# Optimization experiments

Hardware: AMD Instinct MI355X
Metric: run time of the kernel (lower is better)

## Reference

```python
import jax, jax.numpy as jnp
import numpy as np

N = 50000      # nodes
E = 400000     # edges
D = 512        # embed_dim
L = 3          # num gcn layers
INNER = (L + 1) * D
EPS = 1e-5     # BatchNorm1d eps


def setup_inputs() -> dict:
    key = jax.random.key(0)
    ks = jax.random.split(key, 6)
    x = jax.random.normal(ks[0], (N, D), dtype=jnp.float32)
    edge_index = jax.random.randint(ks[1], (2, E), 0, N, dtype=jnp.int64)
    Ws = jax.random.normal(ks[2], (L, D, D), dtype=jnp.float32) / np.float32(np.sqrt(D))
    bs = jnp.zeros((L, D), jnp.float32)
    bn_gamma = jnp.ones((INNER,), jnp.float32)
    bn_beta = jnp.zeros((INNER,), jnp.float32)
    out_W = jax.random.normal(ks[3], (INNER, D), dtype=jnp.float32) / np.float32(np.sqrt(INNER))
    out_b = jnp.zeros((D,), jnp.float32)
    return {"x": x, "edge_index": edge_index, "Ws": Ws, "bs": bs,
            "bn_gamma": bn_gamma, "bn_beta": bn_beta, "out_W": out_W, "out_b": out_b}


def _gcn_conv(x, W, b, src, dst):
    # PyG GCNConv: add self-loops, sym-normalize, aggregate source->target.
    h = x @ W                                            # [N, D]
    deg = jnp.zeros((N,), x.dtype).at[dst].add(1.0) + 1.0  # in-degree + self-loop
    dinv = jax.lax.rsqrt(deg)
    norm = dinv[src] * dinv[dst]                         # [E]
    agg = jnp.zeros_like(h).at[dst].add(h[src] * norm[:, None])
    agg = agg + h * (dinv * dinv)[:, None]               # self-loop messages
    return agg + b


def reference(x, edge_index, Ws, bs, bn_gamma, bn_beta, out_W, out_b):
    src, dst = edge_index[0], edge_index[1]
    h = x
    x_cat = [x]
    for l in range(L):                                   # fixed small layer loop
        h = jax.nn.gelu(_gcn_conv(h, Ws[l], bs[l], src, dst), approximate=False)
        x_cat.append(h)
    xc = jnp.concatenate(x_cat, axis=-1)                 # [N, (L+1)*D]
    # BatchNorm1d, training-mode batch statistics (biased variance)
    mean = jnp.mean(xc, axis=0)
    var = jnp.var(xc, axis=0)
    xn = (xc - mean) * jax.lax.rsqrt(var + EPS) * bn_gamma + bn_beta
    return xn @ out_W + out_b                            # [N, D]
```

## Files before the change

### kernel.cpp

```cpp
#include <hip/hip_runtime.h>
#include <math.h>

#define N_NODES 50000
#define N_EDGES 400000
#define DIM 512
#define NLAYER 3
#define INNER 2048
#define BN_EPS 1e-5f
#define MPAD 50048

typedef unsigned short u16;
typedef unsigned int u32;

typedef __attribute__((ext_vector_type(8))) short bf16x8;
typedef __attribute__((ext_vector_type(4))) float f32x4;

__device__ __forceinline__ u16 f2bf(float f) {
  union { float f; u32 u; } v; v.f = f;
  u32 u = v.u;
  u32 r = (u + 0x7FFFu + ((u >> 16) & 1u)) >> 16;
  return (u16)r;
}
__device__ __forceinline__ float bf2f(u16 h) {
  union { u32 u; float f; } v; v.u = ((u32)h) << 16; return v.f;
}

#define GLOAD_LDS16(g, l)                                                       \
  __builtin_amdgcn_global_load_lds(                                             \
      (const __attribute__((address_space(1))) u32*)(g),                        \
      (__attribute__((address_space(3))) u32*)(l), 16, 0, 0)


__global__ void k_deg(const int* __restrict__ ei, int* __restrict__ deg) {
  int e = blockIdx.x * blockDim.x + threadIdx.x;
  if (e < N_EDGES) atomicAdd(&deg[ei[N_EDGES + e]], 1);
}

__global__ void k_dinv(const int* __restrict__ deg, float* __restrict__ dinv) {
  int i = blockIdx.x * blockDim.x + threadIdx.x;
  if (i < N_NODES) dinv[i] = rsqrtf((float)(deg[i] + 1));
}

__global__ __launch_bounds__(1024) void k_scan1(const int* __restrict__ deg,
                                                int* __restrict__ bsum, int n) {
  __shared__ int wsum[16];
  int tid = threadIdx.x;
  int lane = tid & 63, wv = tid >> 6;
  int i = blockIdx.x * 1024 + tid;
  int x = (i < n) ? deg[i] : 0;
#pragma unroll
  for (int d = 1; d < 64; d <<= 1) x += __shfl_xor(x, d, 64);
  if (lane == 0) wsum[wv] = x;
  __syncthreads();
  if (tid == 0) {
    int s = 0;
#pragma unroll
    for (int k = 0; k < 16; k++) s += wsum[k];
    bsum[blockIdx.x] = s;
  }
}

__global__ void k_scan2(int* __restrict__ bsum, int* __restrict__ offs, int nb) {
  int lane = threadIdx.x;
  int v = (lane < nb) ? bsum[lane] : 0;
  int x = v;
#pragma unroll
  for (int d = 1; d < 64; d <<= 1) {
    int y = __shfl_up(x, d, 64);
    if (lane >= d) x += y;
  }
  if (lane < nb) bsum[lane] = x - v;
  if (lane == nb - 1) offs[N_NODES] = x;
}

__global__ __launch_bounds__(1024) void k_scan3(const int* __restrict__ deg,
                                                const int* __restrict__ bsum,
                                                int* __restrict__ offs, int n) {
  __shared__ int wsum[16];
  int tid = threadIdx.x;
  int lane = tid & 63, wv = tid >> 6;
  int i = blockIdx.x * 1024 + tid;
  int v = (i < n) ? deg[i] : 0;
  int x = v;
#pragma unroll
  for (int d = 1; d < 64; d <<= 1) {
    int y = __shfl_up(x, d, 64);
    if (lane >= d) x += y;
  }
  if (lane == 63) wsum[wv] = x;
  __syncthreads();
  if (wv == 0) {
    int w = (lane < 16) ? wsum[lane] : 0;
#pragma unroll
    for (int d = 1; d < 16; d <<= 1) {
      int y = __shfl_up(w, d, 64);
      if (lane >= d) w += y;
    }
    if (lane < 16) wsum[lane] = w;
  }
  __syncthreads();
  if (i < n) offs[i] = bsum[blockIdx.x] + (wv ? wsum[wv - 1] : 0) + x - v;
}

__global__ void k_fill(const int* __restrict__ ei, const int* __restrict__ offs,
                       int* __restrict__ cursor, const float* __restrict__ dinv,
                       int* __restrict__ csr_src, float* __restrict__ csr_norm) {
  int e = blockIdx.x * blockDim.x + threadIdx.x;
  if (e >= N_EDGES) return;
  int s = ei[e];
  int d = ei[N_EDGES + e];
  int p = atomicAdd(&cursor[d], 1);
  int idx = offs[d] + p;
  csr_src[idx] = s;
  csr_norm[idx] = dinv[s] * dinv[d];
}

__global__ void k_convert(const float* __restrict__ src, u16* __restrict__ xcat, int n4) {
  int i = blockIdx.x * blockDim.x + threadIdx.x;
  if (i >= n4) return;
  float4 v = ((const float4*)src)[i];
  uint2 o;
  o.x = (u32)f2bf(v.x) | ((u32)f2bf(v.y) << 16);
  o.y = (u32)f2bf(v.z) | ((u32)f2bf(v.w) << 16);
  int row = i >> 7;
  int c4 = (i & 127) * 4;
  *(uint2*)(xcat + (size_t)row * INNER + c4) = o;
}

__global__ __launch_bounds__(256) void k_transpose_tiled(
    const float* __restrict__ W, const float* __restrict__ scale,
    u16* __restrict__ WT, int K) {
  __shared__ float tile[32][33];
  int k0 = blockIdx.x * 32, j0 = blockIdx.y * 32;
  int c = threadIdx.x & 31, r8 = threadIdx.x >> 5;
#pragma unroll
  for (int rr = 0; rr < 4; rr++) {
    int row = rr * 8 + r8;
    float v = W[(size_t)(k0 + row) * DIM + j0 + c];
    if (scale) v *= scale[k0 + row];
    tile[row][c] = v;
  }
  __syncthreads();
#pragma unroll
  for (int rr = 0; rr < 4; rr++) {
    int row = rr * 8 + r8;
    WT[(size_t)(j0 + row) * K + k0 + c] = f2bf(tile[c][row]);
  }
}

#define BM 128
#define BN 128
#define BK 32

__global__ __launch_bounds__(256) void gemm_bt(
    const u16* __restrict__ A, int lda,
    const u16* __restrict__ Bt, const float* __restrict__ bias,
    float* __restrict__ Cf, u16* __restrict__ Cb, int M, int K) {
  __shared__ __align__(16) u16 As[BM * BK];
  __shared__ __align__(16) u16 Bs[BN * BK];
  int tid = threadIdx.x;

  int Mblocks = gridDim.y;
  int flat = blockIdx.y * gridDim.x + blockIdx.x;
  int g = flat >> 5;
  int r = flat & 31;
  int P = Mblocks - (g << 3);
  P = (P > 8) ? 8 : P;
  int mb = (g << 3) + r % P;
  int nb = r / P;
  int m0 = mb * BM;
  int n0 = nb * BN;

  int wave = tid >> 6, lane = tid & 63;
  int wm = (wave & 1) * 64, wn = (wave >> 1) * 64;
  int lr = lane & 15;
  int lq = lane >> 4;
  int ric = lane >> 2;
  int seg = (lane & 3) * 8;

  const u16* ap0 = A + (size_t)(m0 + wave * 32 + ric) * lda + seg;
  const u16* ap1 = ap0 + (size_t)16 * lda;
  const u16* bp0 = Bt + (size_t)(n0 + wave * 32 + ric) * K + seg;
  const u16* bp1 = bp0 + (size_t)16 * K;
  u16* asl0 = &As[(wave * 2) * 512];
  u16* asl1 = asl0 + 512;
  u16* bsl0 = &Bs[(wave * 2) * 512];
  u16* bsl1 = bsl0 + 512;

  f32x4 acc[4][4];
#pragma unroll
  for (int i = 0; i < 4; i++)
#pragma unroll
    for (int j = 0; j < 4; j++) acc[i][j] = (f32x4){0.f, 0.f, 0.f, 0.f};

  for (int k0 = 0; k0 < K; k0 += BK) {
    GLOAD_LDS16(ap0, asl0);
    GLOAD_LDS16(ap1, asl1);
    GLOAD_LDS16(bp0, bsl0);
    GLOAD_LDS16(bp1, bsl1);
    ap0 += BK; ap1 += BK; bp0 += BK; bp1 += BK;
    __syncthreads();
    bf16x8 af[4], bfr[4];
#pragma unroll
    for (int i = 0; i < 4; i++)
      af[i] = *(const bf16x8*)(&As[(wm + i * 16 + lr) * BK + lq * 8]);
#pragma unroll
    for (int j = 0; j < 4; j++)
      bfr[j] = *(const bf16x8*)(&Bs[(wn + j * 16 + lr) * BK + lq * 8]);
#pragma unroll
    for (int i = 0; i < 4; i++)
#pragma unroll
      for (int j = 0; j < 4; j++)
        acc[i][j] = __builtin_amdgcn_mfma_f32_16x16x32_bf16(af[i], bfr[j], acc[i][j], 0, 0, 0);
    __syncthreads();
  }
#pragma unroll
  for (int i = 0; i < 4; i++) {
    int row_b = m0 + wm + i * 16 + lq * 4;
#pragma unroll
    for (int j = 0; j < 4; j++) {
      int col = n0 + wn + j * 16 + lr;
      if (Cf) {
        float bv = bias ? bias[col] : 0.f;
#pragma unroll
        for (int r2 = 0; r2 < 4; r2++) {
          int row = row_b + r2;
          if (row < M) Cf[(size_t)row * DIM + col] = acc[i][j][r2] + bv;
        }
      } else {
#pragma unroll
        for (int r2 = 0; r2 < 4; r2++)
          Cb[(size_t)(row_b + r2) * DIM + col] = f2bf(acc[i][j][r2]);
      }
    }
  }
}

__device__ __forceinline__ void accum8(float* a, uint4 h, float w) {
  a[0] += w * bf2f((u16)(h.x & 0xffffu));
  a[1] += w * bf2f((u16)(h.x >> 16));
  a[2] += w * bf2f((u16)(h.y & 0xffffu));
  a[3] += w * bf2f((u16)(h.y >> 16));
  a[4] += w * bf2f((u16)(h.z & 0xffffu));
  a[5] += w * bf2f((u16)(h.z >> 16));
  a[6] += w * bf2f((u16)(h.w & 0xffffu));
  a[7] += w * bf2f((u16)(h.w >> 16));
}

__global__ __launch_bounds__(256) void k_aggregate(
    const u16* __restrict__ hp, const int* __restrict__ offs,
    const int* __restrict__ csr_src, const float* __restrict__ csr_norm,
    const float* __restrict__ dinv, const float* __restrict__ b,
    u16* __restrict__ out_slice) {
  int v = blockIdx.x * 4 + (threadIdx.x >> 6);
  if (v >= N_NODES) return;
  int lane = threadIdx.x & 63;
  int c8 = lane * 8;
  float acc[8];
#pragma unroll
  for (int i = 0; i < 8; i++) acc[i] = 0.f;

  int e0 = offs[v], e1 = offs[v + 1];
  int e = e0;
  for (; e + 4 <= e1; e += 4) {
    int s0 = csr_src[e], s1 = csr_src[e + 1], s2 = csr_src[e + 2], s3 = csr_src[e + 3];
    float w0 = csr_norm[e], w1 = csr_norm[e + 1], w2 = csr_norm[e + 2], w3 = csr_norm[e + 3];
    uint4 h0 = *(const uint4*)(hp + (size_t)s0 * DIM + c8);
    uint4 h1 = *(const uint4*)(hp + (size_t)s1 * DIM + c8);
    uint4 h2 = *(const uint4*)(hp + (size_t)s2 * DIM + c8);
    uint4 h3 = *(const uint4*)(hp + (size_t)s3 * DIM + c8);
    accum8(acc, h0, w0);
    accum8(acc, h1, w1);
    accum8(acc, h2, w2);
    accum8(acc, h3, w3);
  }
  for (; e < e1; e++) {
    int s = csr_src[e];
    float w = csr_norm[e];
    uint4 hv = *(const uint4*)(hp + (size_t)s * DIM + c8);
    accum8(acc, hv, w);
  }
  float di = dinv[v];
  uint4 hv = *(const uint4*)(hp + (size_t)v * DIM + c8);
  accum8(acc, hv, di * di);
  const float4* bb = (const float4*)(b + c8);
  float4 b0 = bb[0], b1 = bb[1];
  acc[0] += b0.x; acc[1] += b0.y; acc[2] += b0.z; acc[3] += b0.w;
  acc[4] += b1.x; acc[5] += b1.y; acc[6] += b1.z; acc[7] += b1.w;
#pragma unroll
  for (int i = 0; i < 8; i++)
    acc[i] = 0.5f * acc[i] * (1.f + erff(acc[i] * 0.70710678118654752f));
  uint4 o;
  o.x = (u32)f2bf(acc[0]) | ((u32)f2bf(acc[1]) << 16);
  o.y = (u32)f2bf(acc[2]) | ((u32)f2bf(acc[3]) << 16);
  o.z = (u32)f2bf(acc[4]) | ((u32)f2bf(acc[5]) << 16);
  o.w = (u32)f2bf(acc[6]) | ((u32)f2bf(acc[7]) << 16);
  *(uint4*)(out_slice + (size_t)v * INNER + c8) = o;
}

__global__ void k_bn_stats(const u16* __restrict__ xcat,
                           float* __restrict__ sums, float* __restrict__ sumsq,
                           int rows_per) {
  int c = blockIdx.x * 512 + threadIdx.x * 2;
  int r0 = blockIdx.y * rows_per;
  int r1 = min(N_NODES, r0 + rows_per);
  float s0 = 0.f, ss0 = 0.f, s1 = 0.f, ss1 = 0.f;
  for (int r = r0; r < r1; r++) {
    u32 u = *(const u32*)(xcat + (size_t)r * INNER + c);
    float x0 = bf2f((u16)(u & 0xffffu));
    float x1 = bf2f((u16)(u >> 16));
    s0 += x0; ss0 += x0 * x0;
    s1 += x1; ss1 += x1 * x1;
  }
  atomicAdd(&sums[c], s0);
  atomicAdd(&sumsq[c], ss0);
  atomicAdd(&sums[c + 1], s1);
  atomicAdd(&sumsq[c + 1], ss1);
}

__global__ void k_bn_finalize(const float* __restrict__ sums, const float* __restrict__ sumsq,
                              const float* __restrict__ gamma, const float* __restrict__ beta,
                              float* __restrict__ scale, float* __restrict__ shift) {
  int c = blockIdx.x * blockDim.x + threadIdx.x;
  if (c >= INNER) return;
  float mean = sums[c] / (float)N_NODES;
  float var = sumsq[c] / (float)N_NODES - mean * mean;
  float rstd = rsqrtf(var + BN_EPS);
  float sc = gamma[c] * rstd;
  scale[c] = sc;
  shift[c] = beta[c] - mean * sc;
}

__global__ __launch_bounds__(256) void k_fold_bias(
    const float* __restrict__ outW, const float* __restrict__ shift,
    const float* __restrict__ outb, float* __restrict__ biasp) {
  int r0 = blockIdx.x * 64;
  int c = threadIdx.x * 2;
  float s0 = 0.f, s1 = 0.f;
  for (int r = 0; r < 64; r++) {
    int row = r0 + r;
    float sh = shift[row];
    float2 w = *(const float2*)(outW + (size_t)row * DIM + c);
    s0 += sh * w.x;
    s1 += sh * w.y;
  }
  if (blockIdx.x == 0) { s0 += outb[c]; s1 += outb[c + 1]; }
  atomicAdd(&biasp[c], s0);
  atomicAdd(&biasp[c + 1], s1);
}

extern "C" void kernel_launch(void* const* d_in, const int* in_sizes, int n_in,
                              void* d_out, int out_size, void* d_ws, size_t ws_size,
                              hipStream_t stream) {
  (void)in_sizes; (void)n_in; (void)out_size; (void)ws_size;
  const float* x     = (const float*)d_in[0];
  const int*   ei    = (const int*)d_in[1];
  const float* Ws    = (const float*)d_in[2];
  const float* bs    = (const float*)d_in[3];
  const float* gamma = (const float*)d_in[4];
  const float* beta  = (const float*)d_in[5];
  const float* outW  = (const float*)d_in[6];
  const float* outb  = (const float*)d_in[7];
  float* out = (float*)d_out;
  u16*   hp  = (u16*)d_out;

  char* ws = (char*)d_ws;
  size_t off = 0;
  auto alloc = [&](size_t bytes) -> void* {
    void* p = ws + off;
    off = (off + bytes + 255) & ~(size_t)255;
    return p;
  };
  int*   deg    = (int*)alloc(N_NODES * 4);
  int*   cursor = (int*)alloc(N_NODES * 4);
  float* sums   = (float*)alloc(INNER * 4);
  float* sumsq  = (float*)alloc(INNER * 4);
  float* biasp  = (float*)alloc(DIM * 4);
  size_t zero_bytes = off;
  float* dinv     = (float*)alloc(N_NODES * 4);
  int*   offs     = (int*)alloc((N_NODES + 1) * 4);
  int*   bsum     = (int*)alloc(64 * 4);
  int*   csr_src  = (int*)alloc(N_EDGES * 4);
  float* csr_norm = (float*)alloc(N_EDGES * 4);
  u16*   xcat = (u16*)alloc((size_t)MPAD * INNER * 2);
  u16*   WbT  = (u16*)alloc((size_t)DIM * DIM * 2);
  u16*   WpT  = (u16*)alloc((size_t)INNER * DIM * 2);
  float* scale = (float*)alloc(INNER * 4);
  float* shift = (float*)alloc(INNER * 4);

  const int SCAN_BLOCKS = (N_NODES + 1023) / 1024;

  hipMemsetAsync(d_ws, 0, zero_bytes, stream);
  k_deg<<<(N_EDGES + 255) / 256, 256, 0, stream>>>(ei, deg);
  k_dinv<<<(N_NODES + 255) / 256, 256, 0, stream>>>(deg, dinv);
  k_scan1<<<SCAN_BLOCKS, 1024, 0, stream>>>(deg, bsum, N_NODES);
  k_scan2<<<1, 64, 0, stream>>>(bsum, offs, SCAN_BLOCKS);
  k_scan3<<<SCAN_BLOCKS, 1024, 0, stream>>>(deg, bsum, offs, N_NODES);
  k_fill<<<(N_EDGES + 255) / 256, 256, 0, stream>>>(ei, offs, cursor, dinv, csr_src, csr_norm);
  k_convert<<<((N_NODES * DIM / 4) + 255) / 256, 256, 0, stream>>>(x, xcat, N_NODES * DIM / 4);

  dim3 ggrid(DIM / BN, MPAD / BM);
  for (int l = 0; l < NLAYER; l++) {
    k_transpose_tiled<<<dim3(DIM / 32, DIM / 32), 256, 0, stream>>>(
        Ws + (size_t)l * DIM * DIM, nullptr, WbT, DIM);
    gemm_bt<<<ggrid, 256, 0, stream>>>(xcat + (size_t)l * DIM, INNER, WbT, nullptr,
                                       nullptr, hp, N_NODES, DIM);
    k_aggregate<<<(N_NODES + 3) / 4, 256, 0, stream>>>(hp, offs, csr_src, csr_norm, dinv,
                                                       bs + (size_t)l * DIM,
                                                       xcat + (size_t)(l + 1) * DIM);
  }
  k_bn_stats<<<dim3(INNER / 512, 125), 256, 0, stream>>>(xcat, sums, sumsq, 400);
  k_bn_finalize<<<INNER / 256, 256, 0, stream>>>(sums, sumsq, gamma, beta, scale, shift);
  k_transpose_tiled<<<dim3(INNER / 32, DIM / 32), 256, 0, stream>>>(outW, scale, WpT, INNER);
  k_fold_bias<<<INNER / 64, 256, 0, stream>>>(outW, shift, outb, biasp);
  gemm_bt<<<ggrid, 256, 0, stream>>>(xcat, INNER, WpT, biasp,
                                     out, nullptr, N_NODES, INNER);
}
```

Measured before the change: 925.1 us.

## Triple-buffer GEMM LDS tiles with async global-to-LDS prefetch pipeline

Replaces the single-buffered GEMM main loop with a three-stage LDS ring buffer. Tiles are prefetched two iterations ahead using direct global-to-LDS loads, with explicit vmcnt waits and barriers, so that global memory latency overlaps the MFMA work. MFMA priority is also raised with s_setprio. The cost is three times the LDS footprint (48 KB), which may lower occupancy, and the hand-written waitcnt sequencing is fragile.

```diff
diff --git a/kernel.cpp b/kernel.cpp
--- a/kernel.cpp
+++ b/kernel.cpp
@@ -151,13 +151,44 @@
 #define BM 128
 #define BN 128
 #define BK 32
+#define TILE_U16 4096
+
+#define GEMM_BODY(VMSTR, DOSTAGE)                                              \
+  {                                                                            \
+    asm volatile("s_waitcnt vmcnt(" VMSTR ")" ::: "memory");                   \
+    asm volatile("s_barrier" ::: "memory");                                    \
+    const u16* asb = As + cur * TILE_U16;                                      \
+    const u16* bsb = Bs + cur * TILE_U16;                                      \
+    bf16x8 af[4], bfr[4];                                                      \
+    _Pragma("unroll") for (int i = 0; i < 4; i++)                              \
+        af[i] = *(const bf16x8*)(asb + (wm + i * 16 + lr) * BK + lq * 8);      \
+    _Pragma("unroll") for (int j = 0; j < 4; j++)                              \
+        bfr[j] = *(const bf16x8*)(bsb + (wn + j * 16 + lr) * BK + lq * 8);     \
+    asm volatile("s_waitcnt lgkmcnt(0)" ::: "memory");                         \
+    __builtin_amdgcn_sched_barrier(0);                                         \
+    asm volatile("s_barrier" ::: "memory");                                    \
+    if (DOSTAGE) {                                                             \
+      GLOAD_LDS16(ap0, asl0 + cur * TILE_U16);                                 \
+      GLOAD_LDS16(ap1, asl1 + cur * TILE_U16);                                 \
+      GLOAD_LDS16(bp0, bsl0 + cur * TILE_U16);                                 \
+      GLOAD_LDS16(bp1, bsl1 + cur * TILE_U16);                                 \
+      ap0 += BK; ap1 += BK; bp0 += BK; bp1 += BK;                              \
+    }                                                                          \
+    __builtin_amdgcn_s_setprio(1);                                             \
+    _Pragma("unroll") for (int i = 0; i < 4; i++)                              \
+      _Pragma("unroll") for (int j = 0; j < 4; j++)                            \
+        acc[i][j] = __builtin_amdgcn_mfma_f32_16x16x32_bf16(af[i], bfr[j],     \
+                                                            acc[i][j], 0, 0, 0); \
+    __builtin_amdgcn_s_setprio(0);                                             \
+    cur = (cur == 2) ? 0 : cur + 1;                                            \
+  }
 
 __global__ __launch_bounds__(256) void gemm_bt(
     const u16* __restrict__ A, int lda,
     const u16* __restrict__ Bt, const float* __restrict__ bias,
     float* __restrict__ Cf, u16* __restrict__ Cb, int M, int K) {
-  __shared__ __align__(16) u16 As[BM * BK];
-  __shared__ __align__(16) u16 Bs[BN * BK];
+  __shared__ __align__(16) u16 As[3 * TILE_U16];
+  __shared__ __align__(16) u16 Bs[3 * TILE_U16];
   int tid = threadIdx.x;
 
   int Mblocks = gridDim.y;
@@ -193,27 +224,21 @@
 #pragma unroll
     for (int j = 0; j < 4; j++) acc[i][j] = (f32x4){0.f, 0.f, 0.f, 0.f};
 
-  for (int k0 = 0; k0 < K; k0 += BK) {
-    GLOAD_LDS16(ap0, asl0);
-    GLOAD_LDS16(ap1, asl1);
-    GLOAD_LDS16(bp0, bsl0);
-    GLOAD_LDS16(bp1, bsl1);
-    ap0 += BK; ap1 += BK; bp0 += BK; bp1 += BK;
-    __syncthreads();
-    bf16x8 af[4], bfr[4];
-#pragma unroll
-    for (int i = 0; i < 4; i++)
-      af[i] = *(const bf16x8*)(&As[(wm + i * 16 + lr) * BK + lq * 8]);
-#pragma unroll
-    for (int j = 0; j < 4; j++)
-      bfr[j] = *(const bf16x8*)(&Bs[(wn + j * 16 + lr) * BK + lq * 8]);
-#pragma unroll
-    for (int i = 0; i < 4; i++)
-#pragma unroll
-      for (int j = 0; j < 4; j++)
-        acc[i][j] = __builtin_amdgcn_mfma_f32_16x16x32_bf16(af[i], bfr[j], acc[i][j], 0, 0, 0);
-    __syncthreads();
-  }
+#pragma unroll
+  for (int s = 0; s < 3; ++s) {
+    GLOAD_LDS16(ap0, asl0 + s * TILE_U16); ap0 += BK;
+    GLOAD_LDS16(ap1, asl1 + s * TILE_U16); ap1 += BK;
+    GLOAD_LDS16(bp0, bsl0 + s * TILE_U16); bp0 += BK;
+    GLOAD_LDS16(bp1, bsl1 + s * TILE_U16); bp1 += BK;
+  }
+
+  int NT = K >> 5;
+  int cur = 0;
+  int t = 0;
+  for (; t < NT - 3; ++t) GEMM_BODY("8", 1);
+  GEMM_BODY("8", 0);
+  GEMM_BODY("4", 0);
+  GEMM_BODY("0", 0);
 #pragma unroll
   for (int i = 0; i < 4; i++) {
     int row_b = m0 + wm + i * 16 + lq * 4;
```

Result: no change. 912.8 us (-1.3%).

## Rewrite GEMM with 256x256 tiles, double-buffered LDS prefetch and 8 waves

Applied to the files above, without the earlier changes.

The bf16 MFMA GEMM moves from 128x128x32 tiles with 4 waves and a single LDS buffer to 256x256x64 tiles with 8 waves, a two-stage double-buffered global-to-LDS pipeline using vmcnt waits, and s_setprio around MFMA bursts. The grid becomes 1D with a swizzled block mapping, and MPAD grows to a multiple of 256. The goal is to hide global load latency behind MFMA work and raise reuse per LDS byte. In exchange it uses far more registers and LDS, so fewer blocks fit per CU, and it launches fewer, larger blocks for the N=512 output.

```diff
diff --git a/kernel.cpp b/kernel.cpp
--- a/kernel.cpp
+++ b/kernel.cpp
@@ -7,7 +7,7 @@
 #define NLAYER 3
 #define INNER 2048
 #define BN_EPS 1e-5f
-#define MPAD 50048
+#define MPAD 50176
 
 typedef unsigned short u16;
 typedef unsigned int u32;
@@ -148,78 +148,111 @@
   }
 }
 
-#define BM 128
-#define BN 128
-#define BK 32
-
-__global__ __launch_bounds__(256) void gemm_bt(
+#define BM 256
+#define BN 256
+#define BK 64
+
+#define STAGE2(t, d)                                                        \
+  {                                                                         \
+    const u16* a_ = aw + (size_t)(t) * 64;                                  \
+    const u16* b_ = bw + (size_t)(t) * 64;                                  \
+    u16* al = aL + (d) * 16384;                                             \
+    u16* bl = bL + (d) * 16384;                                             \
+    GLOAD_LDS16(a_, al);                                                    \
+    GLOAD_LDS16(a_ + (size_t)16 * lda, al + 512);                           \
+    GLOAD_LDS16(a_ + 32, al + 8192);                                        \
+    GLOAD_LDS16(a_ + (size_t)16 * lda + 32, al + 8192 + 512);               \
+    GLOAD_LDS16(b_, bl);                                                    \
+    GLOAD_LDS16(b_ + (size_t)16 * K, bl + 512);                             \
+    GLOAD_LDS16(b_ + 32, bl + 8192);                                        \
+    GLOAD_LDS16(b_ + (size_t)16 * K + 32, bl + 8192 + 512);                 \
+  }
+
+#define TILE_COMPUTE(d)                                                     \
+  {                                                                         \
+    const u16* ab = arp + (d) * 16384;                                      \
+    const u16* bb = brp + (d) * 16384;                                      \
+    bf16x8 af[4][2], bfr[4][2];                                             \
+    _Pragma("unroll") for (int ii = 0; ii < 4; ii++)                        \
+      _Pragma("unroll") for (int s = 0; s < 2; s++)                         \
+        af[ii][s] = *(const bf16x8*)(ab + s * 8192 + ii * 512);             \
+    _Pragma("unroll") for (int j = 0; j < 4; j++)                           \
+      _Pragma("unroll") for (int s = 0; s < 2; s++)                         \
+        bfr[j][s] = *(const bf16x8*)(bb + s * 8192 + j * 512);              \
+    __builtin_amdgcn_s_setprio(1);                                          \
+    _Pragma("unroll") for (int ii = 0; ii < 4; ii++)                        \
+      _Pragma("unroll") for (int j = 0; j < 4; j++)                         \
+        _Pragma("unroll") for (int s = 0; s < 2; s++)                       \
+          acc[ii][j] = __builtin_amdgcn_mfma_f32_16x16x32_bf16(             \
+              af[ii][s], bfr[j][s], acc[ii][j], 0, 0, 0);                   \
+    __builtin_amdgcn_s_setprio(0);                                          \
+    _Pragma("unroll") for (int ii = 0; ii < 4; ii++)                        \
+      _Pragma("unroll") for (int s = 0; s < 2; s++)                         \
+        af[ii][s] = *(const bf16x8*)(ab + s * 8192 + (4 + ii) * 512);       \
+    __builtin_amdgcn_s_setprio(1);                                          \
+    _Pragma("unroll") for (int ii = 0; ii < 4; ii++)                        \
+      _Pragma("unroll") for (int j = 0; j < 4; j++)                         \
+        _Pragma("unroll") for (int s = 0; s < 2; s++)                       \
+          acc[4 + ii][j] = __builtin_amdgcn_mfma_f32_16x16x32_bf16(         \
+              af[ii][s], bfr[j][s], acc[4 + ii][j], 0, 0, 0);               \
+    __builtin_amdgcn_s_setprio(0);                                          \
+  }
+
+__global__ __launch_bounds__(512, 2) void gemm_bt(
     const u16* __restrict__ A, int lda,
     const u16* __restrict__ Bt, const float* __restrict__ bias,
     float* __restrict__ Cf, u16* __restrict__ Cb, int M, int K) {
-  __shared__ __align__(16) u16 As[BM * BK];
-  __shared__ __align__(16) u16 Bs[BN * BK];
+  __shared__ __align__(16) u16 As_[2 * 2 * 256 * 32];
+  __shared__ __align__(16) u16 Bs_[2 * 2 * 256 * 32];
   int tid = threadIdx.x;
-
-  int Mblocks = gridDim.y;
-  int flat = blockIdx.y * gridDim.x + blockIdx.x;
-  int g = flat >> 5;
-  int r = flat & 31;
-  int P = Mblocks - (g << 3);
-  P = (P > 8) ? 8 : P;
-  int mb = (g << 3) + r % P;
-  int nb = r / P;
-  int m0 = mb * BM;
-  int n0 = nb * BN;
-
-  int wave = tid >> 6, lane = tid & 63;
-  int wm = (wave & 1) * 64, wn = (wave >> 1) * 64;
-  int lr = lane & 15;
-  int lq = lane >> 4;
-  int ric = lane >> 2;
-  int seg = (lane & 3) * 8;
-
-  const u16* ap0 = A + (size_t)(m0 + wave * 32 + ric) * lda + seg;
-  const u16* ap1 = ap0 + (size_t)16 * lda;
-  const u16* bp0 = Bt + (size_t)(n0 + wave * 32 + ric) * K + seg;
-  const u16* bp1 = bp0 + (size_t)16 * K;
-  u16* asl0 = &As[(wave * 2) * 512];
-  u16* asl1 = asl0 + 512;
-  u16* bsl0 = &Bs[(wave * 2) * 512];
-  u16* bsl1 = bsl0 + 512;
-
-  f32x4 acc[4][4];
-#pragma unroll
-  for (int i = 0; i < 4; i++)
+  int w = tid >> 6, lane = tid & 63;
+  int wr = w >> 2, wc = w & 3;
+
+  int nwg = gridDim.x;
+  int flat = blockIdx.x;
+  int swz = flat;
+  if ((nwg & 7) == 0) swz = (flat & 7) * (nwg >> 3) + (flat >> 3);
+  int mb = swz >> 1, nb = swz & 1;
+  int m0 = mb * BM, n0 = nb * BN;
+
+  int sr = lane >> 2;
+  int sc = (lane & 3) * 8;
+  const u16* aw = A + (size_t)(m0 + w * 32 + sr) * lda + sc;
+  const u16* bw = Bt + (size_t)(n0 + w * 32 + sr) * K + sc;
+  u16* aL = &As_[(size_t)(w * 32) * 32];
+  u16* bL = &Bs_[(size_t)(w * 32) * 32];
+
+  int lr16 = lane & 15, lq4 = lane >> 4;
+  const u16* arp = &As_[(size_t)(wr * 128 + lr16) * 32 + lq4 * 8];
+  const u16* brp = &Bs_[(size_t)(wc * 64 + lr16) * 32 + lq4 * 8];
+
+  f32x4 acc[8][4];
+#pragma unroll
+  for (int i = 0; i < 8; i++)
 #pragma unroll
     for (int j = 0; j < 4; j++) acc[i][j] = (f32x4){0.f, 0.f, 0.f, 0.f};
 
-  for (int k0 = 0; k0 < K; k0 += BK) {
-    GLOAD_LDS16(ap0, asl0);
-    GLOAD_LDS16(ap1, asl1);
-    GLOAD_LDS16(bp0, bsl0);
-    GLOAD_LDS16(bp1, bsl1);
-    ap0 += BK; ap1 += BK; bp0 += BK; bp1 += BK;
-    __syncthreads();
-    bf16x8 af[4], bfr[4];
-#pragma unroll
-    for (int i = 0; i < 4; i++)
-      af[i] = *(const bf16x8*)(&As[(wm + i * 16 + lr) * BK + lq * 8]);
-#pragma unroll
-    for (int j = 0; j < 4; j++)
-      bfr[j] = *(const bf16x8*)(&Bs[(wn + j * 16 + lr) * BK + lq * 8]);
-#pragma unroll
-    for (int i = 0; i < 4; i++)
-#pragma unroll
-      for (int j = 0; j < 4; j++)
-        acc[i][j] = __builtin_amdgcn_mfma_f32_16x16x32_bf16(af[i], bfr[j], acc[i][j], 0, 0, 0);
-    __syncthreads();
-  }
-#pragma unroll
-  for (int i = 0; i < 4; i++) {
-    int row_b = m0 + wm + i * 16 + lq * 4;
+  STAGE2(0, 0);
+  STAGE2(1, 1);
+
+  int NT = K >> 6;
+  for (int t = 0; t < NT - 1; ++t) {
+    asm volatile("s_waitcnt vmcnt(8)" ::: "memory");
+    __builtin_amdgcn_s_barrier();
+    TILE_COMPUTE(t & 1);
+    __builtin_amdgcn_s_barrier();
+    if (t + 2 < NT) STAGE2(t + 2, t & 1);
+  }
+  asm volatile("s_waitcnt vmcnt(0)" ::: "memory");
+  __builtin_amdgcn_s_barrier();
+  TILE_COMPUTE((NT - 1) & 1);
+
+#pragma unroll
+  for (int i = 0; i < 8; i++) {
+    int row_b = m0 + wr * 128 + i * 16 + lq4 * 4;
 #pragma unroll
     for (int j = 0; j < 4; j++) {
-      int col = n0 + wn + j * 16 + lr;
+      int col = n0 + wc * 64 + j * 16 + lr16;
       if (Cf) {
         float bv = bias ? bias[col] : 0.f;
 #pragma unroll
@@ -399,11 +432,11 @@
   k_fill<<<(N_EDGES + 255) / 256, 256, 0, stream>>>(ei, offs, cursor, dinv, csr_src, csr_norm);
   k_convert<<<((N_NODES * DIM / 4) + 255) / 256, 256, 0, stream>>>(x, xcat, N_NODES * DIM / 4);
 
-  dim3 ggrid(DIM / BN, MPAD / BM);
+  dim3 ggrid((MPAD / BM) * (DIM / BN));
   for (int l = 0; l < NLAYER; l++) {
     k_transpose_tiled<<<dim3(DIM / 32, DIM / 32), 256, 0, stream>>>(
         Ws + (size_t)l * DIM * DIM, nullptr, WbT, DIM);
-    gemm_bt<<<ggrid, 256, 0, stream>>>(xcat + (size_t)l * DIM, INNER, WbT, nullptr,
+    gemm_bt<<<ggrid, 512, 0, stream>>>(xcat + (size_t)l * DIM, INNER, WbT, nullptr,
                                        nullptr, hp, N_NODES, DIM);
     k_aggregate<<<(N_NODES + 3) / 4, 256, 0, stream>>>(hp, offs, csr_src, csr_norm, dinv,
                                                        bs + (size_t)l * DIM,
@@ -413,6 +446,6 @@
   k_bn_finalize<<<INNER / 256, 256, 0, stream>>>(sums, sumsq, gamma, beta, scale, shift);
   k_transpose_tiled<<<dim3(INNER / 32, DIM / 32), 256, 0, stream>>>(outW, scale, WpT, INNER);
   k_fold_bias<<<INNER / 64, 256, 0, stream>>>(outW, shift, outb, biasp);
-  gemm_bt<<<ggrid, 256, 0, stream>>>(xcat, INNER, WpT, biasp,
+  gemm_bt<<<ggrid, 512, 0, stream>>>(xcat, INNER, WpT, biasp,
                                      out, nullptr, N_NODES, INNER);
 }
```

New measurement: 934.0 us. About the same (+1.0%).
